# Kernel optimization log

Hardware: AMD Instinct MI355X
Metric: run time of the kernel (lower is better)

Reference implementation:

```python
import jax, jax.numpy as jnp
import numpy as np

NUM_HEADS = 8
LATENT_FRAME = 4
D_MODEL = 1024
D_FF = 1024  # dim_feedforward == output_dim in the torch module
N_LAYERS = 6
IN_DIM = 128
LN_EPS = 1e-5


def get_slopes(n):
    # standard ALiBi slopes for power-of-two head counts: 2^{-8(i+1)/n}
    return jnp.asarray([2.0 ** (-8.0 * (i + 1) / n) for i in range(n)], jnp.float32)


def alibi_mask(num_heads, T):
    # non-causal ('future') ALiBi: additive bias -slope_h * |i - j|, shape (H, T, T)
    dist = jnp.abs(jnp.arange(T)[:, None] - jnp.arange(T)[None, :]).astype(jnp.float32)
    return -get_slopes(num_heads)[:, None, None] * dist


def layernorm(x, g, b):
    m = jnp.mean(x, axis=-1, keepdims=True)
    v = jnp.mean((x - m) ** 2, axis=-1, keepdims=True)
    return (x - m) * jax.lax.rsqrt(v + LN_EPS) * g + b


def encoder_layer(x, p, mask):
    # torch TransformerEncoderLayer, post-norm, gelu(exact), dropout=0
    B, T, D = x.shape
    H, Dh = NUM_HEADS, D // NUM_HEADS
    qkv = x @ p['in_w'].T + p['in_b']                      # (B,T,3D)
    q, k, v = jnp.split(qkv, 3, axis=-1)
    hsplit = lambda t: t.reshape(B, T, H, Dh).transpose(0, 2, 1, 3)  # (B,H,T,Dh)
    q, k, v = hsplit(q), hsplit(k), hsplit(v)
    scores = jnp.einsum('bhqd,bhkd->bhqk', q, k) / float(np.sqrt(Dh)) + mask[None]
    attn = jax.nn.softmax(scores, axis=-1)
    o = jnp.einsum('bhqk,bhkd->bhqd', attn, v).transpose(0, 2, 1, 3).reshape(B, T, D)
    o = o @ p['out_w'].T + p['out_b']
    x = layernorm(x + o, p['ln1_g'], p['ln1_b'])
    ff = jax.nn.gelu(x @ p['ff1_w'].T + p['ff1_b'], approximate=False) @ p['ff2_w'].T + p['ff2_b']
    return layernorm(x + ff, p['ln2_g'], p['ln2_b'])


def setup_inputs() -> dict:
    key = jax.random.key(0)
    ks = iter(jax.random.split(key, 32))
    s = 0.02
    B, T, F = 8, 2048, IN_DIM
    Fs = F * LATENT_FRAME  # 512
    inp = {
        'x': jax.random.normal(next(ks), (B, T, F), jnp.float32),
        'pre_w': jax.random.normal(next(ks), (D_MODEL, Fs), jnp.float32) * s,
        'pre_b': jnp.zeros((D_MODEL,), jnp.float32),
        'in_w': jax.random.normal(next(ks), (N_LAYERS, 3 * D_MODEL, D_MODEL), jnp.float32) * s,
        'in_b': jnp.zeros((N_LAYERS, 3 * D_MODEL), jnp.float32),
        'out_w': jax.random.normal(next(ks), (N_LAYERS, D_MODEL, D_MODEL), jnp.float32) * s,
        'out_b': jnp.zeros((N_LAYERS, D_MODEL), jnp.float32),
        'ln1_g': jnp.ones((N_LAYERS, D_MODEL), jnp.float32),
        'ln1_b': jnp.zeros((N_LAYERS, D_MODEL), jnp.float32),
        'ff1_w': jax.random.normal(next(ks), (N_LAYERS, D_FF, D_MODEL), jnp.float32) * s,
        'ff1_b': jnp.zeros((N_LAYERS, D_FF), jnp.float32),
        'ff2_w': jax.random.normal(next(ks), (N_LAYERS, D_MODEL, D_FF), jnp.float32) * s,
        'ff2_b': jnp.zeros((N_LAYERS, D_MODEL), jnp.float32),
        'ln2_g': jnp.ones((N_LAYERS, D_MODEL), jnp.float32),
        'ln2_b': jnp.zeros((N_LAYERS, D_MODEL), jnp.float32),
        'post_w': jax.random.normal(next(ks), (D_MODEL, D_MODEL), jnp.float32) * s,
        'post_b': jnp.zeros((D_MODEL,), jnp.float32),
    }
    return inp


def reference(x, pre_w, pre_b, in_w, in_b, out_w, out_b, ln1_g, ln1_b,
              ff1_w, ff1_b, ff2_w, ff2_b, ln2_g, ln2_b, post_w, post_b):
    B, T, F = x.shape
    Tl = T // LATENT_FRAME
    x = x.reshape(B, Tl, F * LATENT_FRAME)
    x = x @ pre_w.T + pre_b                     # (B, Tl, D)
    mask = alibi_mask(NUM_HEADS, Tl)            # (H, Tl, Tl), shared by all batches
    layers = dict(in_w=in_w, in_b=in_b, out_w=out_w, out_b=out_b,
                  ln1_g=ln1_g, ln1_b=ln1_b, ff1_w=ff1_w, ff1_b=ff1_b,
                  ff2_w=ff2_w, ff2_b=ff2_b, ln2_g=ln2_g, ln2_b=ln2_b)
    def step(h, p):
        return encoder_layer(h, p, mask), None
    x, _ = jax.lax.scan(step, x, layers)
    return x @ post_w.T + post_b
```

## Files before the change

### kernel.cpp

```cpp
#include <hip/hip_runtime.h>
#include <hip/hip_bf16.h>

#define B 8
#define TL 512
#define M_ROWS 4096
#define D 1024
#define DFF 1024
#define H 8
#define DH 128
#define NL 6

typedef unsigned short ushort_t;
typedef unsigned int uint_t;
typedef short bf16x8 __attribute__((ext_vector_type(8)));
typedef float f32x4 __attribute__((ext_vector_type(4)));

__device__ __forceinline__ ushort_t f2bf(float f) {
    uint_t u = __float_as_uint(f);
    u += 0x7FFFu + ((u >> 16) & 1u);
    return (ushort_t)(u >> 16);
}
__device__ __forceinline__ float gelu_exact(float x) {
    return 0.5f * x * (1.0f + erff(x * 0.70710678118654752f));
}
__device__ __forceinline__ void gload_lds16(const ushort_t* g, ushort_t* l) {
    __builtin_amdgcn_global_load_lds(
        (const __attribute__((address_space(1))) void*)g,
        (__attribute__((address_space(3))) void*)l, 16, 0, 0);
}

struct CvtArgs {
    const float* s[7];
    ushort_t* d[7];
    int n[7];
};

__global__ __launch_bounds__(256) void cvt_all(CvtArgs a) {
    const int stride = gridDim.x * blockDim.x;
    const int t0 = blockIdx.x * blockDim.x + threadIdx.x;
#pragma unroll
    for (int seg = 0; seg < 7; ++seg) {
        const float* s = a.s[seg];
        ushort_t* d = a.d[seg];
        const int nq = a.n[seg] >> 2;
        for (int i = t0; i < nq; i += stride) {
            float4 v = *(const float4*)(s + (size_t)i * 4);
            ushort4 o;
            o.x = f2bf(v.x); o.y = f2bf(v.y); o.z = f2bf(v.z); o.w = f2bf(v.w);
            *(ushort4*)(d + (size_t)i * 4) = o;
        }
    }
}

#define LDS_SLOT(r, g) (((r) << 2) + ((g) ^ (((r) >> 1) & 3)))

__global__ __launch_bounds__(256) void gemm_n64(
    const ushort_t* __restrict__ A, const ushort_t* __restrict__ W,
    const float* __restrict__ bias, float* __restrict__ Cf,
    ushort_t* __restrict__ Cb, int M, int N, int K, int do_gelu) {
    __shared__ ushort_t As[128 * 32];
    __shared__ ushort_t Bs[64 * 32];

    const int tid = threadIdx.x;
    const int lane = tid & 63;
    const int w = tid >> 6;
    const int wm = (w & 2) * 32;
    const int wn = (w & 1) * 32;
    const int bm = blockIdx.y * 128;
    const int bn = blockIdx.x * 64;

    const int sA0 = tid, sA1 = tid + 256, sB = tid;
    const int rA0 = sA0 >> 2, gA0c = (sA0 & 3) ^ ((rA0 >> 1) & 3);
    const int rA1 = sA1 >> 2, gA1c = (sA1 & 3) ^ ((rA1 >> 1) & 3);
    const int rB = sB >> 2, gBc = (sB & 3) ^ ((rB >> 1) & 3);
    const ushort_t* gA0 = A + (size_t)(bm + rA0) * K + gA0c * 8;
    const ushort_t* gA1 = A + (size_t)(bm + rA1) * K + gA1c * 8;
    const ushort_t* gB0 = W + (size_t)(bn + rB) * K + gBc * 8;
    ushort_t* lA0 = &As[sA0 * 8];
    ushort_t* lA1 = &As[sA1 * 8];
    ushort_t* lB0 = &Bs[sB * 8];

    const int fr = lane & 15;
    const int fq = lane >> 4;
    int aoff[4], boff[2];
#pragma unroll
    for (int t = 0; t < 4; ++t) aoff[t] = LDS_SLOT(wm + t * 16 + fr, fq) * 8;
#pragma unroll
    for (int t = 0; t < 2; ++t) boff[t] = LDS_SLOT(wn + t * 16 + fr, fq) * 8;

    f32x4 acc[4][2];
#pragma unroll
    for (int i = 0; i < 4; ++i)
#pragma unroll
        for (int j = 0; j < 2; ++j) acc[i][j] = (f32x4){0.f, 0.f, 0.f, 0.f};

    for (int k0 = 0; k0 < K; k0 += 32) {
        gload_lds16(gA0 + k0, lA0);
        gload_lds16(gA1 + k0, lA1);
        gload_lds16(gB0 + k0, lB0);
        __syncthreads();

        bf16x8 af[4], bf[2];
#pragma unroll
        for (int t = 0; t < 4; ++t) af[t] = *(const bf16x8*)&As[aoff[t]];
#pragma unroll
        for (int t = 0; t < 2; ++t) bf[t] = *(const bf16x8*)&Bs[boff[t]];
#pragma unroll
        for (int i = 0; i < 4; ++i)
#pragma unroll
            for (int j = 0; j < 2; ++j)
                acc[i][j] = __builtin_amdgcn_mfma_f32_16x16x32_bf16(
                    af[i], bf[j], acc[i][j], 0, 0, 0);
        __syncthreads();
    }

#pragma unroll
    for (int tj = 0; tj < 2; ++tj) {
        const int n = bn + wn + tj * 16 + fr;
        const float bv = bias[n];
#pragma unroll
        for (int ti = 0; ti < 4; ++ti) {
            const int m0 = bm + wm + ti * 16 + fq * 4;
            f32x4 a = acc[ti][tj];
#pragma unroll
            for (int r = 0; r < 4; ++r) {
                float v = a[r] + bv;
                if (do_gelu) v = gelu_exact(v);
                const size_t off = (size_t)(m0 + r) * N + n;
                if (Cf) Cf[off] = v;
                if (Cb) Cb[off] = f2bf(v);
            }
        }
    }
}

__global__ __launch_bounds__(256) void gemm_qkv(
    const ushort_t* __restrict__ A, const ushort_t* __restrict__ W,
    const float* __restrict__ bias, ushort_t* __restrict__ Qb,
    ushort_t* __restrict__ Kb, ushort_t* __restrict__ Vt, int K) {
    __shared__ ushort_t As[128 * 32];
    __shared__ ushort_t Bs[128 * 32];

    const int tid = threadIdx.x;
    const int lane = tid & 63;
    const int w = tid >> 6;
    const int wm = (w >> 1) * 64;
    const int wn = (w & 1) * 64;
    const int bm = blockIdx.y * 128;
    const int bn = blockIdx.x * 128;

    const int s0 = tid, s1 = tid + 256;
    const int r0 = s0 >> 2, g0 = (s0 & 3) ^ ((r0 >> 1) & 3);
    const int r1 = s1 >> 2, g1 = (s1 & 3) ^ ((r1 >> 1) & 3);
    const ushort_t* gA0 = A + (size_t)(bm + r0) * K + g0 * 8;
    const ushort_t* gA1 = A + (size_t)(bm + r1) * K + g1 * 8;
    const ushort_t* gB0 = W + (size_t)(bn + r0) * K + g0 * 8;
    const ushort_t* gB1 = W + (size_t)(bn + r1) * K + g1 * 8;
    ushort_t* lA0 = &As[s0 * 8];
    ushort_t* lA1 = &As[s1 * 8];
    ushort_t* lB0 = &Bs[s0 * 8];
    ushort_t* lB1 = &Bs[s1 * 8];

    const int fr = lane & 15;
    const int fq = lane >> 4;
    int aoff[4], boff[4];
#pragma unroll
    for (int t = 0; t < 4; ++t) {
        aoff[t] = LDS_SLOT(wm + t * 16 + fr, fq) * 8;
        boff[t] = LDS_SLOT(wn + t * 16 + fr, fq) * 8;
    }

    f32x4 acc[4][4];
#pragma unroll
    for (int i = 0; i < 4; ++i)
#pragma unroll
        for (int j = 0; j < 4; ++j) acc[i][j] = (f32x4){0.f, 0.f, 0.f, 0.f};

    for (int k0 = 0; k0 < K; k0 += 32) {
        gload_lds16(gA0 + k0, lA0);
        gload_lds16(gA1 + k0, lA1);
        gload_lds16(gB0 + k0, lB0);
        gload_lds16(gB1 + k0, lB1);
        __syncthreads();

        bf16x8 af[4], bf[4];
#pragma unroll
        for (int t = 0; t < 4; ++t) af[t] = *(const bf16x8*)&As[aoff[t]];
#pragma unroll
        for (int t = 0; t < 4; ++t) bf[t] = *(const bf16x8*)&Bs[boff[t]];
#pragma unroll
        for (int i = 0; i < 4; ++i)
#pragma unroll
            for (int j = 0; j < 4; ++j)
                acc[i][j] = __builtin_amdgcn_mfma_f32_16x16x32_bf16(
                    af[i], bf[j], acc[i][j], 0, 0, 0);
        __syncthreads();
    }

    const float qscale = 0.08838834764831845f;
#pragma unroll
    for (int tj = 0; tj < 4; ++tj) {
        const int n = bn + wn + tj * 16 + fr;
        const float bv = bias[n];
#pragma unroll
        for (int ti = 0; ti < 4; ++ti) {
            const int m0 = bm + wm + ti * 16 + fq * 4;
            f32x4 a = acc[ti][tj];
            if (n < D) {
#pragma unroll
                for (int r = 0; r < 4; ++r)
                    Qb[(size_t)(m0 + r) * D + n] = f2bf((a[r] + bv) * qscale);
            } else if (n < 2 * D) {
#pragma unroll
                for (int r = 0; r < 4; ++r)
                    Kb[(size_t)(m0 + r) * D + (n - D)] = f2bf(a[r] + bv);
            } else {
                const int h = (n - 2 * D) >> 7;
                const int dh = (n - 2 * D) & 127;
                const int bb = m0 >> 9;
                const int t = m0 & 511;
                ushort4 pk;
                pk.x = f2bf(a[0] + bv); pk.y = f2bf(a[1] + bv);
                pk.z = f2bf(a[2] + bv); pk.w = f2bf(a[3] + bv);
                *(ushort4*)&Vt[((size_t)(bb * H + h) * DH + dh) * TL + t] = pk;
            }
        }
    }
}

#define LSW16(r, g) ((((r) << 4) + ((g) ^ ((r) & 7))) << 3)
#define LSW8(r, g) ((((r) << 3) + ((g) ^ ((r) & 7))) << 3)

__global__ __launch_bounds__(256, 2) void attn_mfma(
    const ushort_t* __restrict__ Qb, const ushort_t* __restrict__ Kb,
    const ushort_t* __restrict__ Vt, ushort_t* __restrict__ Ab) {
    __shared__ ushort_t Qs[64 * 128];
    __shared__ ushort_t Ks[64 * 128];
    __shared__ ushort_t Vts[128 * 64];
    __shared__ ushort_t Ps[64 * 72];

    const int q0 = blockIdx.x * 64;
    const int bh = blockIdx.y;
    const int b = bh >> 3;
    const int h = bh & 7;
    const int tid = threadIdx.x;
    const int lane = tid & 63;
    const int w = tid >> 6;
    const int fr = lane & 15;
    const int fq = lane >> 4;

    const float slope = exp2f(-(float)(h + 1));

#pragma unroll
    for (int kk = 0; kk < 4; ++kk) {
        int s = tid + kk * 256;
        int r = s >> 4, gp = s & 15, gl = gp ^ (r & 7);
        gload_lds16(Qb + (size_t)(b * TL + q0 + r) * D + h * DH + gl * 8,
                    &Qs[s * 8]);
    }

    f32x4 o8[8];
    float m_i[4], l_i[4];
#pragma unroll
    for (int nt = 0; nt < 8; ++nt) o8[nt] = (f32x4){0.f, 0.f, 0.f, 0.f};
#pragma unroll
    for (int r = 0; r < 4; ++r) { m_i[r] = -1e30f; l_i[r] = 0.f; }

    for (int kt = 0; kt < TL / 64; ++kt) {
        __syncthreads();
#pragma unroll
        for (int kk = 0; kk < 4; ++kk) {
            int s = tid + kk * 256;
            int r = s >> 4, gp = s & 15, gl = gp ^ (r & 7);
            gload_lds16(Kb + (size_t)(b * TL + kt * 64 + r) * D + h * DH + gl * 8,
                        &Ks[s * 8]);
        }
#pragma unroll
        for (int kk = 0; kk < 4; ++kk) {
            int s = tid + kk * 256;
            int r = s >> 3, gp = s & 7, gl = gp ^ (r & 7);
            gload_lds16(Vt + ((size_t)bh * DH + r) * TL + kt * 64 + gl * 8,
                        &Vts[s * 8]);
        }
        __syncthreads();

        f32x4 sacc[4];
#pragma unroll
        for (int jt = 0; jt < 4; ++jt) sacc[jt] = (f32x4){0.f, 0.f, 0.f, 0.f};
#pragma unroll
        for (int s4 = 0; s4 < 4; ++s4) {
            bf16x8 aq = *(const bf16x8*)&Qs[LSW16(w * 16 + fr, s4 * 4 + fq)];
#pragma unroll
            for (int jt = 0; jt < 4; ++jt) {
                bf16x8 kb = *(const bf16x8*)&Ks[LSW16(jt * 16 + fr, s4 * 4 + fq)];
                sacc[jt] = __builtin_amdgcn_mfma_f32_16x16x32_bf16(
                    aq, kb, sacc[jt], 0, 0, 0);
            }
        }

        const int iq = q0 + w * 16 + fq * 4;
        const int jk = kt * 64 + fr;
        float al[4];
#pragma unroll
        for (int r = 0; r < 4; ++r) {
            float sv[4];
#pragma unroll
            for (int jt = 0; jt < 4; ++jt)
                sv[jt] = sacc[jt][r] -
                         slope * fabsf((float)(iq + r - jk - jt * 16));
            float mx = fmaxf(fmaxf(sv[0], sv[1]), fmaxf(sv[2], sv[3]));
            mx = fmaxf(mx, __shfl_xor(mx, 1));
            mx = fmaxf(mx, __shfl_xor(mx, 2));
            mx = fmaxf(mx, __shfl_xor(mx, 4));
            mx = fmaxf(mx, __shfl_xor(mx, 8));
            float mnew = fmaxf(m_i[r], mx);
            al[r] = __expf(m_i[r] - mnew);
            float rs = 0.f;
#pragma unroll
            for (int jt = 0; jt < 4; ++jt) {
                sv[jt] = __expf(sv[jt] - mnew);
                rs += sv[jt];
            }
            rs += __shfl_xor(rs, 1);
            rs += __shfl_xor(rs, 2);
            rs += __shfl_xor(rs, 4);
            rs += __shfl_xor(rs, 8);
            l_i[r] = l_i[r] * al[r] + rs;
            m_i[r] = mnew;
            const int prow = w * 16 + fq * 4 + r;
#pragma unroll
            for (int jt = 0; jt < 4; ++jt)
                Ps[prow * 72 + jt * 16 + fr] = f2bf(sv[jt]);
        }
#pragma unroll
        for (int nt = 0; nt < 8; ++nt)
#pragma unroll
            for (int r = 0; r < 4; ++r) o8[nt][r] *= al[r];

#pragma unroll
        for (int s2 = 0; s2 < 2; ++s2) {
            bf16x8 pa = *(const bf16x8*)&Ps[(w * 16 + fr) * 72 + s2 * 32 + fq * 8];
#pragma unroll
            for (int nt = 0; nt < 8; ++nt) {
                bf16x8 vb = *(const bf16x8*)&Vts[LSW8(nt * 16 + fr, s2 * 4 + fq)];
                o8[nt] = __builtin_amdgcn_mfma_f32_16x16x32_bf16(
                    pa, vb, o8[nt], 0, 0, 0);
            }
        }
    }

#pragma unroll
    for (int r = 0; r < 4; ++r) {
        float inv = 1.f / l_i[r];
        const size_t base = (size_t)(b * TL + q0 + w * 16 + fq * 4 + r) * D + h * DH;
#pragma unroll
        for (int nt = 0; nt < 8; ++nt)
            Ab[base + nt * 16 + fr] = f2bf(o8[nt][r] * inv);
    }
}

__global__ __launch_bounds__(256) void add_ln(const float* __restrict__ x,
                                              const float* __restrict__ y,
                                              const float* __restrict__ g,
                                              const float* __restrict__ bta,
                                              float* __restrict__ out,
                                              ushort_t* __restrict__ outb) {
    __shared__ float red[4];
    const int row = blockIdx.x;
    const int tid = threadIdx.x;
    const size_t base = (size_t)row * D + tid * 4;

    float4 xv = *(const float4*)(x + base);
    float4 yv = *(const float4*)(y + base);
    float v[4] = {xv.x + yv.x, xv.y + yv.y, xv.z + yv.z, xv.w + yv.w};

    float s = v[0] + v[1] + v[2] + v[3];
    for (int off = 32; off; off >>= 1) s += __shfl_down(s, off);
    if ((tid & 63) == 0) red[tid >> 6] = s;
    __syncthreads();
    const float mean = (red[0] + red[1] + red[2] + red[3]) * (1.f / (float)D);
    __syncthreads();

    float d0 = v[0] - mean, d1 = v[1] - mean, d2 = v[2] - mean, d3 = v[3] - mean;
    float sq = d0 * d0 + d1 * d1 + d2 * d2 + d3 * d3;
    for (int off = 32; off; off >>= 1) sq += __shfl_down(sq, off);
    if ((tid & 63) == 0) red[tid >> 6] = sq;
    __syncthreads();
    const float var = (red[0] + red[1] + red[2] + red[3]) * (1.f / (float)D);
    const float inv = rsqrtf(var + 1e-5f);

    float4 gv = *(const float4*)(g + tid * 4);
    float4 bv = *(const float4*)(bta + tid * 4);
    float4 o;
    o.x = d0 * inv * gv.x + bv.x;
    o.y = d1 * inv * gv.y + bv.y;
    o.z = d2 * inv * gv.z + bv.z;
    o.w = d3 * inv * gv.w + bv.w;
    *(float4*)(out + base) = o;
    ushort4 ob;
    ob.x = f2bf(o.x); ob.y = f2bf(o.y); ob.z = f2bf(o.z); ob.w = f2bf(o.w);
    *(ushort4*)(outb + base) = ob;
}

extern "C" void kernel_launch(void* const* d_in, const int* in_sizes, int n_in,
                              void* d_out, int out_size, void* d_ws, size_t ws_size,
                              hipStream_t stream) {
    const float* x_in   = (const float*)d_in[0];
    const float* pre_w  = (const float*)d_in[1];
    const float* pre_b  = (const float*)d_in[2];
    const float* in_w   = (const float*)d_in[3];
    const float* in_b   = (const float*)d_in[4];
    const float* out_w  = (const float*)d_in[5];
    const float* out_b  = (const float*)d_in[6];
    const float* ln1_g  = (const float*)d_in[7];
    const float* ln1_b  = (const float*)d_in[8];
    const float* ff1_w  = (const float*)d_in[9];
    const float* ff1_b  = (const float*)d_in[10];
    const float* ff2_w  = (const float*)d_in[11];
    const float* ff2_b  = (const float*)d_in[12];
    const float* ln2_g  = (const float*)d_in[13];
    const float* ln2_b  = (const float*)d_in[14];
    const float* post_w = (const float*)d_in[15];
    const float* post_b = (const float*)d_in[16];

    float* X = (float*)d_ws;
    float* Y = X + (size_t)M_ROWS * D;
    ushort_t* Xb   = (ushort_t*)(Y + (size_t)M_ROWS * D);
    ushort_t* Ab   = Xb + (size_t)M_ROWS * D;
    ushort_t* Qb   = Ab + (size_t)M_ROWS * D;
    ushort_t* Kb   = Qb + (size_t)M_ROWS * D;
    ushort_t* Vt   = Kb + (size_t)M_ROWS * D;
    ushort_t* xinb = Vt + (size_t)M_ROWS * D;
    ushort_t* pwb  = xinb + (size_t)M_ROWS * 512;
    ushort_t* iwb  = pwb + (size_t)D * 512;
    ushort_t* owb  = iwb + (size_t)NL * 3 * D * D;
    ushort_t* f1wb = owb + (size_t)NL * D * D;
    ushort_t* f2wb = f1wb + (size_t)NL * DFF * D;
    ushort_t* powb = f2wb + (size_t)NL * D * DFF;

    const dim3 blk(256);

    CvtArgs ca;
    ca.s[0] = x_in;   ca.d[0] = xinb; ca.n[0] = M_ROWS * 512;
    ca.s[1] = pre_w;  ca.d[1] = pwb;  ca.n[1] = D * 512;
    ca.s[2] = in_w;   ca.d[2] = iwb;  ca.n[2] = NL * 3 * D * D;
    ca.s[3] = out_w;  ca.d[3] = owb;  ca.n[3] = NL * D * D;
    ca.s[4] = ff1_w;  ca.d[4] = f1wb; ca.n[4] = NL * DFF * D;
    ca.s[5] = ff2_w;  ca.d[5] = f2wb; ca.n[5] = NL * D * DFF;
    ca.s[6] = post_w; ca.d[6] = powb; ca.n[6] = D * D;
    cvt_all<<<1024, blk, 0, stream>>>(ca);

    const dim3 gN64(D / 64, M_ROWS / 128);
    const dim3 gQKV(3 * D / 128, M_ROWS / 128);

    gemm_n64<<<gN64, blk, 0, stream>>>(xinb, pwb, pre_b, X, Xb,
                                       M_ROWS, D, 512, 0);

    for (int l = 0; l < NL; ++l) {
        gemm_qkv<<<gQKV, blk, 0, stream>>>(Xb, iwb + (size_t)l * 3 * D * D,
                                           in_b + (size_t)l * 3 * D,
                                           Qb, Kb, Vt, D);
        attn_mfma<<<dim3(TL / 64, B * H), blk, 0, stream>>>(Qb, Kb, Vt, Ab);
        gemm_n64<<<gN64, blk, 0, stream>>>(Ab, owb + (size_t)l * D * D,
                                           out_b + (size_t)l * D, Y, nullptr,
                                           M_ROWS, D, D, 0);
        add_ln<<<dim3(M_ROWS), blk, 0, stream>>>(X, Y, ln1_g + (size_t)l * D,
                                                 ln1_b + (size_t)l * D, X, Xb);
        gemm_n64<<<gN64, blk, 0, stream>>>(Xb, f1wb + (size_t)l * DFF * D,
                                           ff1_b + (size_t)l * DFF, nullptr, Ab,
                                           M_ROWS, DFF, D, 1);
        gemm_n64<<<gN64, blk, 0, stream>>>(Ab, f2wb + (size_t)l * D * DFF,
                                           ff2_b + (size_t)l * D, Y, nullptr,
                                           M_ROWS, D, DFF, 0);
        add_ln<<<dim3(M_ROWS), blk, 0, stream>>>(X, Y, ln2_g + (size_t)l * D,
                                                 ln2_b + (size_t)l * D, X, Xb);
    }

    gemm_n64<<<gN64, blk, 0, stream>>>(Xb, powb, post_b, (float*)d_out, nullptr,
                                       M_ROWS, D, D, 0);
}
```

Measured before the change: 1.215 ms.

## Double GEMM K-tile to 64 with 8-way swizzle and rebalance conversion kernel

Both GEMM kernels now stage a 64-wide K slice per iteration into LDS, using a new 8-column XOR swizzle, and issue two MFMA sub-steps per sync pair. This halves the number of barrier round trips and global-load issue phases per output tile. The cost is doubled LDS per block, which may lower occupancy. Separately, the weight conversion kernel now gives each segment a proportional range of blocks and launches 4096 blocks instead of 1024 with a grid-stride loop over every segment.

```diff
diff --git a/kernel.cpp b/kernel.cpp
--- a/kernel.cpp
+++ b/kernel.cpp
@@ -32,18 +32,21 @@
 struct CvtArgs {
     const float* s[7];
     ushort_t* d[7];
-    int n[7];
+    int nq[7];
+    int bstart[8];
 };
 
 __global__ __launch_bounds__(256) void cvt_all(CvtArgs a) {
-    const int stride = gridDim.x * blockDim.x;
-    const int t0 = blockIdx.x * blockDim.x + threadIdx.x;
+    const int bid = blockIdx.x;
 #pragma unroll
     for (int seg = 0; seg < 7; ++seg) {
+        const int b0 = a.bstart[seg], b1 = a.bstart[seg + 1];
+        if (bid < b0 || bid >= b1) continue;
+        const int stride = (b1 - b0) * 256;
         const float* s = a.s[seg];
         ushort_t* d = a.d[seg];
-        const int nq = a.n[seg] >> 2;
-        for (int i = t0; i < nq; i += stride) {
+        const int nq = a.nq[seg];
+        for (int i = (bid - b0) * 256 + threadIdx.x; i < nq; i += stride) {
             float4 v = *(const float4*)(s + (size_t)i * 4);
             ushort4 o;
             o.x = f2bf(v.x); o.y = f2bf(v.y); o.z = f2bf(v.z); o.w = f2bf(v.w);
@@ -52,14 +55,14 @@
     }
 }
 
-#define LDS_SLOT(r, g) (((r) << 2) + ((g) ^ (((r) >> 1) & 3)))
+#define LSLOT64(r, c) (((r) * 8 + ((c) ^ ((r) & 7))) * 8)
 
 __global__ __launch_bounds__(256) void gemm_n64(
     const ushort_t* __restrict__ A, const ushort_t* __restrict__ W,
     const float* __restrict__ bias, float* __restrict__ Cf,
     ushort_t* __restrict__ Cb, int M, int N, int K, int do_gelu) {
-    __shared__ ushort_t As[128 * 32];
-    __shared__ ushort_t Bs[64 * 32];
+    __shared__ ushort_t As[128 * 64];
+    __shared__ ushort_t Bs[64 * 64];
 
     const int tid = threadIdx.x;
     const int lane = tid & 63;
@@ -69,24 +72,38 @@
     const int bm = blockIdx.y * 128;
     const int bn = blockIdx.x * 64;
 
-    const int sA0 = tid, sA1 = tid + 256, sB = tid;
-    const int rA0 = sA0 >> 2, gA0c = (sA0 & 3) ^ ((rA0 >> 1) & 3);
-    const int rA1 = sA1 >> 2, gA1c = (sA1 & 3) ^ ((rA1 >> 1) & 3);
-    const int rB = sB >> 2, gBc = (sB & 3) ^ ((rB >> 1) & 3);
-    const ushort_t* gA0 = A + (size_t)(bm + rA0) * K + gA0c * 8;
-    const ushort_t* gA1 = A + (size_t)(bm + rA1) * K + gA1c * 8;
-    const ushort_t* gB0 = W + (size_t)(bn + rB) * K + gBc * 8;
-    ushort_t* lA0 = &As[sA0 * 8];
-    ushort_t* lA1 = &As[sA1 * 8];
-    ushort_t* lB0 = &Bs[sB * 8];
+    const ushort_t* gA[4];
+    ushort_t* lA[4];
+#pragma unroll
+    for (int t = 0; t < 4; ++t) {
+        int s = tid + t * 256;
+        int r = s >> 3, gl = (s & 7) ^ (r & 7);
+        gA[t] = A + (size_t)(bm + r) * K + gl * 8;
+        lA[t] = &As[s * 8];
+    }
+    const ushort_t* gB[2];
+    ushort_t* lB[2];
+#pragma unroll
+    for (int t = 0; t < 2; ++t) {
+        int s = tid + t * 256;
+        int r = s >> 3, gl = (s & 7) ^ (r & 7);
+        gB[t] = W + (size_t)(bn + r) * K + gl * 8;
+        lB[t] = &Bs[s * 8];
+    }
 
     const int fr = lane & 15;
     const int fq = lane >> 4;
-    int aoff[4], boff[2];
-#pragma unroll
-    for (int t = 0; t < 4; ++t) aoff[t] = LDS_SLOT(wm + t * 16 + fr, fq) * 8;
-#pragma unroll
-    for (int t = 0; t < 2; ++t) boff[t] = LDS_SLOT(wn + t * 16 + fr, fq) * 8;
+    int aoff[4][2], boff[2][2];
+#pragma unroll
+    for (int t = 0; t < 4; ++t)
+#pragma unroll
+        for (int s = 0; s < 2; ++s)
+            aoff[t][s] = LSLOT64(wm + t * 16 + fr, s * 4 + fq);
+#pragma unroll
+    for (int t = 0; t < 2; ++t)
+#pragma unroll
+        for (int s = 0; s < 2; ++s)
+            boff[t][s] = LSLOT64(wn + t * 16 + fr, s * 4 + fq);
 
     f32x4 acc[4][2];
 #pragma unroll
@@ -94,23 +111,27 @@
 #pragma unroll
         for (int j = 0; j < 2; ++j) acc[i][j] = (f32x4){0.f, 0.f, 0.f, 0.f};
 
-    for (int k0 = 0; k0 < K; k0 += 32) {
-        gload_lds16(gA0 + k0, lA0);
-        gload_lds16(gA1 + k0, lA1);
-        gload_lds16(gB0 + k0, lB0);
+    for (int k0 = 0; k0 < K; k0 += 64) {
+#pragma unroll
+        for (int t = 0; t < 4; ++t) gload_lds16(gA[t] + k0, lA[t]);
+#pragma unroll
+        for (int t = 0; t < 2; ++t) gload_lds16(gB[t] + k0, lB[t]);
         __syncthreads();
 
-        bf16x8 af[4], bf[2];
-#pragma unroll
-        for (int t = 0; t < 4; ++t) af[t] = *(const bf16x8*)&As[aoff[t]];
-#pragma unroll
-        for (int t = 0; t < 2; ++t) bf[t] = *(const bf16x8*)&Bs[boff[t]];
-#pragma unroll
-        for (int i = 0; i < 4; ++i)
-#pragma unroll
-            for (int j = 0; j < 2; ++j)
-                acc[i][j] = __builtin_amdgcn_mfma_f32_16x16x32_bf16(
-                    af[i], bf[j], acc[i][j], 0, 0, 0);
+#pragma unroll
+        for (int s = 0; s < 2; ++s) {
+            bf16x8 af[4], bf[2];
+#pragma unroll
+            for (int t = 0; t < 4; ++t) af[t] = *(const bf16x8*)&As[aoff[t][s]];
+#pragma unroll
+            for (int t = 0; t < 2; ++t) bf[t] = *(const bf16x8*)&Bs[boff[t][s]];
+#pragma unroll
+            for (int i = 0; i < 4; ++i)
+#pragma unroll
+                for (int j = 0; j < 2; ++j)
+                    acc[i][j] = __builtin_amdgcn_mfma_f32_16x16x32_bf16(
+                        af[i], bf[j], acc[i][j], 0, 0, 0);
+        }
         __syncthreads();
     }
 
@@ -138,8 +159,8 @@
     const ushort_t* __restrict__ A, const ushort_t* __restrict__ W,
     const float* __restrict__ bias, ushort_t* __restrict__ Qb,
     ushort_t* __restrict__ Kb, ushort_t* __restrict__ Vt, int K) {
-    __shared__ ushort_t As[128 * 32];
-    __shared__ ushort_t Bs[128 * 32];
+    __shared__ ushort_t As[128 * 64];
+    __shared__ ushort_t Bs[128 * 64];
 
     const int tid = threadIdx.x;
     const int lane = tid & 63;
@@ -149,26 +170,30 @@
     const int bm = blockIdx.y * 128;
     const int bn = blockIdx.x * 128;
 
-    const int s0 = tid, s1 = tid + 256;
-    const int r0 = s0 >> 2, g0 = (s0 & 3) ^ ((r0 >> 1) & 3);
-    const int r1 = s1 >> 2, g1 = (s1 & 3) ^ ((r1 >> 1) & 3);
-    const ushort_t* gA0 = A + (size_t)(bm + r0) * K + g0 * 8;
-    const ushort_t* gA1 = A + (size_t)(bm + r1) * K + g1 * 8;
-    const ushort_t* gB0 = W + (size_t)(bn + r0) * K + g0 * 8;
-    const ushort_t* gB1 = W + (size_t)(bn + r1) * K + g1 * 8;
-    ushort_t* lA0 = &As[s0 * 8];
-    ushort_t* lA1 = &As[s1 * 8];
-    ushort_t* lB0 = &Bs[s0 * 8];
-    ushort_t* lB1 = &Bs[s1 * 8];
+    const ushort_t* gA[4];
+    const ushort_t* gB[4];
+    ushort_t* lA[4];
+    ushort_t* lB[4];
+#pragma unroll
+    for (int t = 0; t < 4; ++t) {
+        int s = tid + t * 256;
+        int r = s >> 3, gl = (s & 7) ^ (r & 7);
+        gA[t] = A + (size_t)(bm + r) * K + gl * 8;
+        gB[t] = W + (size_t)(bn + r) * K + gl * 8;
+        lA[t] = &As[s * 8];
+        lB[t] = &Bs[s * 8];
+    }
 
     const int fr = lane & 15;
     const int fq = lane >> 4;
-    int aoff[4], boff[4];
-#pragma unroll
-    for (int t = 0; t < 4; ++t) {
-        aoff[t] = LDS_SLOT(wm + t * 16 + fr, fq) * 8;
-        boff[t] = LDS_SLOT(wn + t * 16 + fr, fq) * 8;
-    }
+    int aoff[4][2], boff[4][2];
+#pragma unroll
+    for (int t = 0; t < 4; ++t)
+#pragma unroll
+        for (int s = 0; s < 2; ++s) {
+            aoff[t][s] = LSLOT64(wm + t * 16 + fr, s * 4 + fq);
+            boff[t][s] = LSLOT64(wn + t * 16 + fr, s * 4 + fq);
+        }
 
     f32x4 acc[4][4];
 #pragma unroll
@@ -176,24 +201,27 @@
 #pragma unroll
         for (int j = 0; j < 4; ++j) acc[i][j] = (f32x4){0.f, 0.f, 0.f, 0.f};
 
-    for (int k0 = 0; k0 < K; k0 += 32) {
-        gload_lds16(gA0 + k0, lA0);
-        gload_lds16(gA1 + k0, lA1);
-        gload_lds16(gB0 + k0, lB0);
-        gload_lds16(gB1 + k0, lB1);
+    for (int k0 = 0; k0 < K; k0 += 64) {
+#pragma unroll
+        for (int t = 0; t < 4; ++t) gload_lds16(gA[t] + k0, lA[t]);
+#pragma unroll
+        for (int t = 0; t < 4; ++t) gload_lds16(gB[t] + k0, lB[t]);
         __syncthreads();
 
-        bf16x8 af[4], bf[4];
-#pragma unroll
-        for (int t = 0; t < 4; ++t) af[t] = *(const bf16x8*)&As[aoff[t]];
-#pragma unroll
-        for (int t = 0; t < 4; ++t) bf[t] = *(const bf16x8*)&Bs[boff[t]];
-#pragma unroll
-        for (int i = 0; i < 4; ++i)
-#pragma unroll
-            for (int j = 0; j < 4; ++j)
-                acc[i][j] = __builtin_amdgcn_mfma_f32_16x16x32_bf16(
-                    af[i], bf[j], acc[i][j], 0, 0, 0);
+#pragma unroll
+        for (int s = 0; s < 2; ++s) {
+            bf16x8 af[4], bf[4];
+#pragma unroll
+            for (int t = 0; t < 4; ++t) af[t] = *(const bf16x8*)&As[aoff[t][s]];
+#pragma unroll
+            for (int t = 0; t < 4; ++t) bf[t] = *(const bf16x8*)&Bs[boff[t][s]];
+#pragma unroll
+            for (int i = 0; i < 4; ++i)
+#pragma unroll
+                for (int j = 0; j < 4; ++j)
+                    acc[i][j] = __builtin_amdgcn_mfma_f32_16x16x32_bf16(
+                        af[i], bf[j], acc[i][j], 0, 0, 0);
+        }
         __syncthreads();
     }
 
@@ -441,14 +469,25 @@
     const dim3 blk(256);
 
     CvtArgs ca;
-    ca.s[0] = x_in;   ca.d[0] = xinb; ca.n[0] = M_ROWS * 512;
-    ca.s[1] = pre_w;  ca.d[1] = pwb;  ca.n[1] = D * 512;
-    ca.s[2] = in_w;   ca.d[2] = iwb;  ca.n[2] = NL * 3 * D * D;
-    ca.s[3] = out_w;  ca.d[3] = owb;  ca.n[3] = NL * D * D;
-    ca.s[4] = ff1_w;  ca.d[4] = f1wb; ca.n[4] = NL * DFF * D;
-    ca.s[5] = ff2_w;  ca.d[5] = f2wb; ca.n[5] = NL * D * DFF;
-    ca.s[6] = post_w; ca.d[6] = powb; ca.n[6] = D * D;
-    cvt_all<<<1024, blk, 0, stream>>>(ca);
+    ca.s[0] = x_in;   ca.d[0] = xinb; ca.nq[0] = (M_ROWS * 512) / 4;
+    ca.s[1] = pre_w;  ca.d[1] = pwb;  ca.nq[1] = (D * 512) / 4;
+    ca.s[2] = in_w;   ca.d[2] = iwb;  ca.nq[2] = (NL * 3 * D * D) / 4;
+    ca.s[3] = out_w;  ca.d[3] = owb;  ca.nq[3] = (NL * D * D) / 4;
+    ca.s[4] = ff1_w;  ca.d[4] = f1wb; ca.nq[4] = (NL * DFF * D) / 4;
+    ca.s[5] = ff2_w;  ca.d[5] = f2wb; ca.nq[5] = (NL * D * DFF) / 4;
+    ca.s[6] = post_w; ca.d[6] = powb; ca.nq[6] = (D * D) / 4;
+    {
+        long long total = 0;
+        for (int i = 0; i < 7; ++i) total += ca.nq[i];
+        long long cum = 0;
+        ca.bstart[0] = 0;
+        for (int i = 0; i < 7; ++i) {
+            cum += ca.nq[i];
+            ca.bstart[i + 1] = (int)((cum * 4096) / total);
+        }
+        ca.bstart[7] = 4096;
+    }
+    cvt_all<<<4096, blk, 0, stream>>>(ca);
 
     const dim3 gN64(D / 64, M_ROWS / 128);
     const dim3 gQKV(3 * D / 128, M_ROWS / 128);
```

New measurement: 1.148 ms. 1.06x faster.
